# Kernel tuning notes

Measured on AMD Instinct MI355X. Metric: run time of the kernel, lower is better.

The kernel has to match this reference:

```python
import jax, jax.numpy as jnp
import numpy as np

B, S, D = 4, 2048, 1024


def setup_inputs() -> dict:
    key = jax.random.key(0)
    kq, k1, k2, k3 = jax.random.split(key, 4)
    w_scale = 1.0 / np.sqrt(D)  # ~ glorot scale for square Dense
    q = jax.random.normal(kq, (B, S, D), dtype=jnp.float32)
    Wq = jax.random.normal(k1, (D, D), dtype=jnp.float32) * w_scale
    Wk = jax.random.normal(k2, (D, D), dtype=jnp.float32) * w_scale  # unused in self-attn path (bug in original)
    Wv = jax.random.normal(k3, (D, D), dtype=jnp.float32) * w_scale
    # causal mask: 1 = masked (future), matching tf.where(mask == 1, -1e9, scores)
    mask = jnp.triu(jnp.ones((S, S), dtype=jnp.int32), k=1)
    return {"q": q, "Wq": Wq, "Wk": Wk, "Wv": Wv, "mask": mask}


def reference(q, Wq, Wk, Wv, mask):
    # Self-attention path of the original: k=None, v=None.
    WQ = jnp.einsum('bsd,de->bse', q, Wq)
    # Faithful to the original code: dense_v is applied for BOTH K and V.
    WKV = jnp.einsum('bsd,de->bse', q, Wv)
    d_k = jnp.asarray(D, dtype=q.dtype)
    scores = jnp.einsum('bqd,bkd->bqk', WQ, WKV) / jnp.sqrt(d_k)  # [B,S,S]
    scores = jnp.where(mask == 1, jnp.asarray(-1e9, scores.dtype), scores)
    attn = jax.nn.softmax(scores, axis=-1)
    return jnp.einsum('bqk,bkd->bqd', attn, WKV)
```

## Files before the change

### kernel.cpp

```cpp
#include <hip/hip_runtime.h>


typedef unsigned short u16;
typedef short short8 __attribute__((ext_vector_type(8)));
typedef float floatx4 __attribute__((ext_vector_type(4)));

#define S_LEN 2048
#define D_DIM 1024
#define BK 64

__device__ inline u16 f2b(float f) {
  unsigned u = __float_as_uint(f);
  return (u16)((u + 0x7fffu + ((u >> 16) & 1u)) >> 16);
}

__device__ __forceinline__ void gload16(const u16* g, u16* l) {
  __builtin_amdgcn_global_load_lds(
      (const __attribute__((address_space(1))) void*)g,
      (__attribute__((address_space(3))) void*)l, 16, 0, 0);
}

__global__ __launch_bounds__(256)
void cvt_f32_bf16(const float* __restrict__ src, u16* __restrict__ dst) {
  size_t idx = ((size_t)blockIdx.x * 256 + threadIdx.x) * 8;
  float4 a0 = *(const float4*)&src[idx];
  float4 a1 = *(const float4*)&src[idx + 4];
  short8 v;
  v[0] = (short)f2b(a0.x); v[1] = (short)f2b(a0.y);
  v[2] = (short)f2b(a0.z); v[3] = (short)f2b(a0.w);
  v[4] = (short)f2b(a1.x); v[5] = (short)f2b(a1.y);
  v[6] = (short)f2b(a1.z); v[7] = (short)f2b(a1.w);
  *(short8*)&dst[idx] = v;
}

__global__ __launch_bounds__(256)
void transpose_cvt2(const float* __restrict__ s0, u16* __restrict__ d0_,
                    const float* __restrict__ s1, u16* __restrict__ d1_) {
  __shared__ u16 tile[32][33];
  const float* src = blockIdx.z ? s1 : s0;
  u16* dst = blockIdx.z ? d1_ : d0_;
  int c0 = blockIdx.x * 32, r0 = blockIdx.y * 32;
  int tx = threadIdx.x, ty = threadIdx.y;
  for (int ii = 0; ii < 32; ii += 8)
    tile[ii + ty][tx] = f2b(src[(size_t)(r0 + ii + ty) * 1024 + (c0 + tx)]);
  __syncthreads();
  for (int ii = 0; ii < 32; ii += 8)
    dst[(size_t)(c0 + ii + ty) * 1024 + (r0 + tx)] = tile[tx][ii + ty];
}

__global__ __launch_bounds__(256)
void gemm_proj(const u16* __restrict__ A, const u16* __restrict__ B0,
               const u16* __restrict__ B1, u16* __restrict__ C0,
               u16* __restrict__ C1, u16* __restrict__ WKVt) {
  int id = blockIdx.x;
  int xcd = id & 7, i = id >> 3;
  int m_idx = xcd * 8 + (i & 7);
  int nz = i >> 3;
  int n0 = (nz & 7) * 128, z = nz >> 3;
  int m0 = m_idx * 128;
  const u16* Bp = z ? B1 : B0;
  u16* Cp = z ? C1 : C0;
  __shared__ __align__(16) char smem[34816];
  u16* Als = (u16*)smem;
  u16* Bls = (u16*)(smem + 16384);
  u16* Tls = (u16*)smem;
  int tid = threadIdx.x;
  int wave = tid >> 6, lane = tid & 63, quad = lane >> 4, l15 = lane & 15;
  int wm = (wave >> 1) * 64, wn = (wave & 1) * 64;
  int arow = lane >> 3;
  int acol = ((lane & 7) ^ (arow & 7)) << 3;
  floatx4 acc[4][4];
#pragma unroll
  for (int ii = 0; ii < 4; ++ii)
#pragma unroll
    for (int j = 0; j < 4; ++j) acc[ii][j] = (floatx4){0.f, 0.f, 0.f, 0.f};
  for (int kb = 0; kb < D_DIM; kb += BK) {
    __syncthreads();
#pragma unroll
    for (int p = 0; p < 4; ++p) {
      int r0 = p * 32 + wave * 8;
      gload16(&A[(size_t)(m0 + r0 + arow) * D_DIM + kb + acol], &Als[r0 * BK]);
      gload16(&Bp[(size_t)(n0 + r0 + arow) * D_DIM + kb + acol], &Bls[r0 * BK]);
    }
    __syncthreads();
#pragma unroll
    for (int kk8 = 0; kk8 < 8; kk8 += 4) {
      int cg = (((kk8 + quad) & 7) ^ (l15 & 7)) << 3;
      short8 af[4], bfr[4];
#pragma unroll
      for (int ii = 0; ii < 4; ++ii)
        af[ii] = *(const short8*)&Als[(wm + ii * 16 + l15) * BK + cg];
#pragma unroll
      for (int j = 0; j < 4; ++j)
        bfr[j] = *(const short8*)&Bls[(wn + j * 16 + l15) * BK + cg];
#pragma unroll
      for (int ii = 0; ii < 4; ++ii)
#pragma unroll
        for (int j = 0; j < 4; ++j)
          acc[ii][j] = __builtin_amdgcn_mfma_f32_16x16x32_bf16(
              af[ii], bfr[j], acc[ii][j], 0, 0, 0);
    }
  }
#pragma unroll
  for (int ii = 0; ii < 4; ++ii)
#pragma unroll
    for (int j = 0; j < 4; ++j)
#pragma unroll
      for (int r = 0; r < 4; ++r)
        Cp[(size_t)(m0 + wm + ii * 16 + quad * 4 + r) * D_DIM +
           (n0 + wn + j * 16 + l15)] = f2b(acc[ii][j][r]);
  if (z) {
    __syncthreads();
#pragma unroll
    for (int ii = 0; ii < 4; ++ii)
#pragma unroll
      for (int j = 0; j < 4; ++j)
#pragma unroll
        for (int r = 0; r < 4; ++r)
          Tls[(wn + j * 16 + l15) * 136 + (wm + ii * 16 + quad * 4 + r)] =
              f2b(acc[ii][j][r]);
    __syncthreads();
    int b = m0 >> 11, srow = m0 & 2047;
    u16* Wt = WKVt + (size_t)b * D_DIM * S_LEN;
#pragma unroll
    for (int p = 0; p < 8; ++p) {
      int e = p * 2048 + tid * 8;
      int d = e >> 7, s = e & 127;
      *(short8*)&Wt[(size_t)(n0 + d) * S_LEN + srow + s] =
          *(const short8*)&Tls[d * 136 + s];
    }
  }
}

#define GEMM64_PROLOG()                                                       \
  __shared__ u16 Als[64 * BK];                                                \
  __shared__ u16 Bls[128 * BK];                                               \
  int tid = threadIdx.x;                                                      \
  int wave = tid >> 6, lane = tid & 63, quad = lane >> 4, l15 = lane & 15;    \
  int wr = (wave >> 1) * 32, wc = (wave & 1) * 64;                            \
  int arow = lane >> 3;                                                       \
  int acol = ((lane & 7) ^ (arow & 7)) << 3;                                  \
  floatx4 acc[2][4];                                                          \
  _Pragma("unroll") for (int i = 0; i < 2; ++i)                               \
  _Pragma("unroll") for (int j = 0; j < 4; ++j)                               \
      acc[i][j] = (floatx4){0.f, 0.f, 0.f, 0.f};

#define GEMM64_KLOOP(Aptr, lda, Bptr, ldb, KEND)                              \
  for (int kb = 0; kb < (KEND); kb += BK) {                                   \
    __syncthreads();                                                          \
    _Pragma("unroll") for (int p = 0; p < 2; ++p) {                           \
      int r0 = wave * 16 + p * 8;                                             \
      gload16(&(Aptr)[(size_t)(m0 + r0 + arow) * (lda) + kb + acol],          \
              &Als[r0 * BK]);                                                 \
    }                                                                         \
    _Pragma("unroll") for (int p = 0; p < 4; ++p) {                           \
      int r0 = wave * 32 + p * 8;                                             \
      gload16(&(Bptr)[(size_t)(n0 + r0 + arow) * (ldb) + kb + acol],          \
              &Bls[r0 * BK]);                                                 \
    }                                                                         \
    __syncthreads();                                                          \
    _Pragma("unroll") for (int kk8 = 0; kk8 < 8; kk8 += 4) {                  \
      int cg = (((kk8 + quad) & 7) ^ (l15 & 7)) << 3;                         \
      short8 af[2], bfr[4];                                                   \
      _Pragma("unroll") for (int i = 0; i < 2; ++i)                           \
          af[i] = *(const short8*)&Als[(wr + i * 16 + l15) * BK + cg];        \
      _Pragma("unroll") for (int j = 0; j < 4; ++j)                           \
          bfr[j] = *(const short8*)&Bls[(wc + j * 16 + l15) * BK + cg];       \
      _Pragma("unroll") for (int i = 0; i < 2; ++i)                           \
      _Pragma("unroll") for (int j = 0; j < 4; ++j)                           \
          acc[i][j] = __builtin_amdgcn_mfma_f32_16x16x32_bf16(                \
              af[i], bfr[j], acc[i][j], 0, 0, 0);                             \
    }                                                                         \
  }

__global__ __launch_bounds__(256)
void gemm_scores(const u16* __restrict__ WQ, const u16* __restrict__ WKV,
                 u16* __restrict__ Pp, float* __restrict__ rowsum) {
  int id = blockIdx.x;
  int xcd = id & 7;
  int b = xcd & 3, h = xcd >> 2;
  int t = id >> 3;
  int m = (int)((sqrtf(8.f * (float)t + 1.f) - 1.f) * 0.5f);
  while ((m + 1) * (m + 2) / 2 <= t) ++m;
  while (m * (m + 1) / 2 > t) --m;
  int bj = t - m * (m + 1) / 2;
  int bi = 2 * m + h;
  int m0 = bi * 64, n0 = bj * 128;
  const u16* A = WQ + (size_t)b * S_LEN * D_DIM;
  const u16* Bp = WKV + (size_t)b * S_LEN * D_DIM;
  GEMM64_PROLOG();
  GEMM64_KLOOP(A, D_DIM, Bp, D_DIM, D_DIM);
  u16* Pb = Pp + (size_t)b * S_LEN * S_LEN;
  float part[2][4];
#pragma unroll
  for (int i = 0; i < 2; ++i)
#pragma unroll
    for (int r = 0; r < 4; ++r) part[i][r] = 0.f;
#pragma unroll
  for (int i = 0; i < 2; ++i)
#pragma unroll
    for (int j = 0; j < 4; ++j) {
      int col = n0 + wc + j * 16 + l15;
#pragma unroll
      for (int r = 0; r < 4; ++r) {
        int row = m0 + wr + i * 16 + quad * 4 + r;
        float p = (col > row) ? 0.f : __expf(acc[i][j][r] * 0.03125f);
        Pb[(size_t)row * S_LEN + col] = f2b(p);
        part[i][r] += p;
      }
    }
#pragma unroll
  for (int i = 0; i < 2; ++i)
#pragma unroll
    for (int r = 0; r < 4; ++r) {
      float v = part[i][r];
#pragma unroll
      for (int off = 1; off < 16; off <<= 1) v += __shfl_xor(v, off, 64);
      part[i][r] = v;
    }
  if (l15 == 0) {
#pragma unroll
    for (int i = 0; i < 2; ++i)
#pragma unroll
      for (int r = 0; r < 4; ++r)
        atomicAdd(&rowsum[b * S_LEN + m0 + wr + i * 16 + quad * 4 + r],
                  part[i][r]);
  }
}

__global__ __launch_bounds__(256)
void gemm_pv(const u16* __restrict__ Pp, const u16* __restrict__ WKVt,
             const float* __restrict__ rowsum, float* __restrict__ out) {
  int id = blockIdx.x;
  int xcd = id & 7;
  int b = xcd & 3, h = xcd >> 2;
  int r_ = id >> 3;
  int mh = 15 - (r_ >> 3);
  int bi = 2 * mh + h;
  int bj = r_ & 7;
  int m0 = bi * 64, n0 = bj * 128;
  int kend = (bi + 1) * 64;
  const u16* A = Pp + (size_t)b * S_LEN * S_LEN;
  const u16* Bp = WKVt + (size_t)b * (size_t)D_DIM * S_LEN;
  GEMM64_PROLOG();
  GEMM64_KLOOP(A, S_LEN, Bp, S_LEN, kend);
  const float* rs = rowsum + b * S_LEN;
  float* Co = out + (size_t)b * S_LEN * D_DIM;
#pragma unroll
  for (int i = 0; i < 2; ++i)
#pragma unroll
    for (int r = 0; r < 4; ++r) {
      int row = m0 + wr + i * 16 + quad * 4 + r;
      float inv = 1.0f / rs[row];
#pragma unroll
      for (int j = 0; j < 4; ++j)
        Co[(size_t)row * D_DIM + (n0 + wc + j * 16 + l15)] =
            acc[i][j][r] * inv;
    }
}

extern "C" void kernel_launch(void* const* d_in, const int* in_sizes, int n_in,
                              void* d_out, int out_size, void* d_ws, size_t ws_size,
                              hipStream_t stream) {
  const float* q = (const float*)d_in[0];
  const float* Wq = (const float*)d_in[1];
  const float* Wv = (const float*)d_in[3];
  char* ws = (char*)d_ws;
  const size_t MB = 1024 * 1024;
  u16* Wqt = (u16*)(ws);
  u16* Wvt = (u16*)(ws + 2 * MB);
  u16* qb16 = (u16*)(ws + 4 * MB);
  u16* Pp = (u16*)(ws);
  u16* WQ = (u16*)(ws + 32 * MB);
  u16* WKV = (u16*)(ws + 48 * MB);
  u16* WKVt = (u16*)(ws + 64 * MB);
  float* rowsum = (float*)(ws + 80 * MB);

  hipMemsetAsync(rowsum, 0, 4 * S_LEN * sizeof(float), stream);
  cvt_f32_bf16<<<4096, 256, 0, stream>>>(q, qb16);
  transpose_cvt2<<<dim3(32, 32, 2), dim3(32, 8), 0, stream>>>(Wq, Wqt, Wv, Wvt);
  gemm_proj<<<1024, 256, 0, stream>>>(qb16, Wqt, Wvt, WQ, WKV, WKVt);
  gemm_scores<<<1088, 256, 0, stream>>>(WQ, WKV, Pp, rowsum);
  gemm_pv<<<1024, 256, 0, stream>>>(Pp, WKVt, rowsum, (float*)d_out);
}
```

Baseline: 216.8 us.

## Rewrite projection GEMM as 256x256 8-wave tile with pipelined LDS staging

The projection GEMM moves from 128x128 tiles with 4 waves to 256x256 tiles with 8 waves (512 threads, 256 blocks). It uses a 128KB LDS buffer split into eight staged half-tiles, with loads for the next k-step issued while MFMAs on the current data run. Explicit barriers, waitcnt and setprio interleave memory and compute. The aim is more operand reuse per block and hidden global-load latency, at the cost of fewer blocks (256 across the machine, one per CU), heavy register use for the 8x4 accumulators, and a more fragile hand-written schedule.

New measurement: 232.0 us. 1.07x slower.

```diff
diff --git a/kernel.cpp b/kernel.cpp
--- a/kernel.cpp
+++ b/kernel.cpp
@@ -48,86 +48,168 @@
     dst[(size_t)(c0 + ii + ty) * 1024 + (r0 + tx)] = tile[tx][ii + ty];
 }
 
-__global__ __launch_bounds__(256)
+__global__ __launch_bounds__(512)
 void gemm_proj(const u16* __restrict__ A, const u16* __restrict__ B0,
                const u16* __restrict__ B1, u16* __restrict__ C0,
                u16* __restrict__ C1, u16* __restrict__ WKVt) {
+  __shared__ __align__(16) u16 lds[65536];
+
   int id = blockIdx.x;
-  int xcd = id & 7, i = id >> 3;
-  int m_idx = xcd * 8 + (i & 7);
-  int nz = i >> 3;
-  int n0 = (nz & 7) * 128, z = nz >> 3;
-  int m0 = m_idx * 128;
+  int xcd = id & 7, i5 = id >> 3;
+  int m_idx = xcd * 4 + (i5 & 3);
+  int n_idx = i5 >> 2;
+  int z = n_idx >> 2;
+  int n0 = (n_idx & 3) * 256;
+  int m0 = m_idx * 256;
   const u16* Bp = z ? B1 : B0;
   u16* Cp = z ? C1 : C0;
-  __shared__ __align__(16) char smem[34816];
-  u16* Als = (u16*)smem;
-  u16* Bls = (u16*)(smem + 16384);
-  u16* Tls = (u16*)smem;
+
   int tid = threadIdx.x;
-  int wave = tid >> 6, lane = tid & 63, quad = lane >> 4, l15 = lane & 15;
-  int wm = (wave >> 1) * 64, wn = (wave & 1) * 64;
-  int arow = lane >> 3;
-  int acol = ((lane & 7) ^ (arow & 7)) << 3;
-  floatx4 acc[4][4];
-#pragma unroll
-  for (int ii = 0; ii < 4; ++ii)
-#pragma unroll
-    for (int j = 0; j < 4; ++j) acc[ii][j] = (floatx4){0.f, 0.f, 0.f, 0.f};
-  for (int kb = 0; kb < D_DIM; kb += BK) {
-    __syncthreads();
-#pragma unroll
-    for (int p = 0; p < 4; ++p) {
-      int r0 = p * 32 + wave * 8;
-      gload16(&A[(size_t)(m0 + r0 + arow) * D_DIM + kb + acol], &Als[r0 * BK]);
-      gload16(&Bp[(size_t)(n0 + r0 + arow) * D_DIM + kb + acol], &Bls[r0 * BK]);
-    }
-    __syncthreads();
-#pragma unroll
-    for (int kk8 = 0; kk8 < 8; kk8 += 4) {
-      int cg = (((kk8 + quad) & 7) ^ (l15 & 7)) << 3;
-      short8 af[4], bfr[4];
-#pragma unroll
-      for (int ii = 0; ii < 4; ++ii)
-        af[ii] = *(const short8*)&Als[(wm + ii * 16 + l15) * BK + cg];
-#pragma unroll
-      for (int j = 0; j < 4; ++j)
-        bfr[j] = *(const short8*)&Bls[(wn + j * 16 + l15) * BK + cg];
-#pragma unroll
-      for (int ii = 0; ii < 4; ++ii)
-#pragma unroll
-        for (int j = 0; j < 4; ++j)
-          acc[ii][j] = __builtin_amdgcn_mfma_f32_16x16x32_bf16(
-              af[ii], bfr[j], acc[ii][j], 0, 0, 0);
-    }
-  }
-#pragma unroll
-  for (int ii = 0; ii < 4; ++ii)
-#pragma unroll
-    for (int j = 0; j < 4; ++j)
+  int wv = tid >> 6, lane = tid & 63, quad = lane >> 4, l15 = lane & 15;
+  int wm = wv >> 2, wn = wv & 3;
+
+  int off_g[2];
+#pragma unroll
+  for (int l = 0; l < 2; ++l) {
+    int chunk = (wv * 2 + l) * 64 + lane;
+    int r = chunk >> 3, cs = chunk & 7;
+    off_g[l] = r * 1024 + (cs ^ (r & 7)) * 8;
+  }
+  const u16* As0 = A + (size_t)m0 * 1024;
+  const u16* As1 = A + (size_t)(m0 + 128) * 1024;
+  const u16* Bs0 = Bp + (size_t)n0 * 1024;
+  const u16* Bs1 = Bp + (size_t)(n0 + 128) * 1024;
+
+#define PSTAGE(src, reg)                                                     \
+  {                                                                          \
+    _Pragma("unroll") for (int l = 0; l < 2; ++l)                            \
+        gload16((src) + off_g[l], &lds[(reg) * 8192 + (wv * 2 + l) * 512]);  \
+  }
+
+  int aoff[2], boff[2];
+#pragma unroll
+  for (int kk = 0; kk < 2; ++kk) {
+    int c = ((kk * 4 + quad) ^ (l15 & 7)) * 8;
+    aoff[kk] = l15 * 64 + c;
+    boff[kk] = ((wn & 1) * 64 + l15) * 64 + c;
+  }
+  const u16* A0p = &lds[(0 + wm) * 8192];
+  const u16* A1p = &lds[(4 + wm) * 8192];
+  const u16* B0p = &lds[(2 + (wn >> 1)) * 8192];
+  const u16* B1p = &lds[(6 + (wn >> 1)) * 8192];
+
+  floatx4 acc[8][4];
+#pragma unroll
+  for (int i = 0; i < 8; ++i)
+#pragma unroll
+    for (int j = 0; j < 4; ++j) acc[i][j] = (floatx4){0.f, 0.f, 0.f, 0.f};
+
+#define BARp() __builtin_amdgcn_s_barrier()
+#define WLG() asm volatile("s_waitcnt lgkmcnt(0)" ::: "memory")
+#define WVM(n) asm volatile("s_waitcnt vmcnt(" #n ")" ::: "memory")
+
+#define RDA(dst, base, fb)                                                 \
+  _Pragma("unroll") for (int f = 0; f < 4; ++f)                            \
+  _Pragma("unroll") for (int kk = 0; kk < 2; ++kk)                         \
+      dst[f][kk] = *(const short8*)&(base)[((fb) + f) * 1024 + aoff[kk]];
+#define RDB(dst, base, fb)                                                 \
+  _Pragma("unroll") for (int f = 0; f < 2; ++f)                            \
+  _Pragma("unroll") for (int kk = 0; kk < 2; ++kk)                         \
+      dst[f][kk] = *(const short8*)&(base)[((fb) + f) * 1024 + boff[kk]];
+#define MMQ(mh, nh, afq, bfq)                                              \
+  __builtin_amdgcn_s_setprio(1);                                           \
+  _Pragma("unroll") for (int f = 0; f < 4; ++f)                            \
+  _Pragma("unroll") for (int g2 = 0; g2 < 2; ++g2)                         \
+  _Pragma("unroll") for (int kk = 0; kk < 2; ++kk)                         \
+      acc[(mh) * 4 + f][(nh) * 2 + g2] =                                   \
+          __builtin_amdgcn_mfma_f32_16x16x32_bf16(                         \
+              afq[f][kk], bfq[g2][kk], acc[(mh) * 4 + f][(nh) * 2 + g2],   \
+              0, 0, 0);                                                    \
+  __builtin_amdgcn_s_setprio(0);
+
+  PSTAGE(As0, 0); PSTAGE(As1, 1); PSTAGE(Bs0, 2); PSTAGE(Bs1, 3);
+  PSTAGE(As0 + 64, 4); PSTAGE(As1 + 64, 5);
+  WVM(4);
+  BARp();
+
+#pragma unroll 1
+  for (int it = 0; it < 8; ++it) {
+    int kb = it * 128;
+    short8 af0[4][2], af1[4][2], bf0[2][2], bf1[2][2];
+    RDA(af0, A0p, 0); RDB(bf0, B0p, 0);
+    PSTAGE(Bs0 + kb + 64, 6);
+    BARp(); WLG();
+    MMQ(0, 0, af0, bf0);
+    BARp();
+    RDA(af1, A0p, 4); RDB(bf1, B0p, 2);
+    PSTAGE(Bs1 + kb + 64, 7);
+    BARp(); WLG();
+    MMQ(1, 1, af1, bf1);
+    BARp();
+    if (it < 7) PSTAGE(As0 + kb + 128, 0);
+    BARp();
+    MMQ(0, 1, af0, bf1);
+    BARp();
+    if (it < 7) PSTAGE(As1 + kb + 128, 1);
+    BARp();
+    MMQ(1, 0, af1, bf0);
+    if (it < 7) { WVM(4); } else { WVM(0); }
+    BARp();
+    RDA(af0, A1p, 0); RDB(bf0, B1p, 0);
+    if (it < 7) PSTAGE(Bs0 + kb + 128, 2);
+    BARp(); WLG();
+    MMQ(0, 0, af0, bf0);
+    BARp();
+    RDA(af1, A1p, 4); RDB(bf1, B1p, 2);
+    if (it < 7) PSTAGE(Bs1 + kb + 128, 3);
+    BARp(); WLG();
+    MMQ(1, 1, af1, bf1);
+    BARp();
+    if (it < 7) PSTAGE(As0 + kb + 192, 4);
+    BARp();
+    MMQ(0, 1, af0, bf1);
+    BARp();
+    if (it < 7) PSTAGE(As1 + kb + 192, 5);
+    BARp();
+    MMQ(1, 0, af1, bf0);
+    if (it < 7) WVM(4);
+    BARp();
+  }
+
+  asm volatile("s_waitcnt vmcnt(0) lgkmcnt(0)" ::: "memory");
+#pragma unroll
+  for (int mf = 0; mf < 8; ++mf)
+#pragma unroll
+    for (int nf = 0; nf < 4; ++nf)
 #pragma unroll
       for (int r = 0; r < 4; ++r)
-        Cp[(size_t)(m0 + wm + ii * 16 + quad * 4 + r) * D_DIM +
-           (n0 + wn + j * 16 + l15)] = f2b(acc[ii][j][r]);
+        Cp[(size_t)(m0 + wm * 128 + mf * 16 + quad * 4 + r) * D_DIM +
+           (n0 + wn * 64 + nf * 16 + l15)] = f2b(acc[mf][nf][r]);
+
   if (z) {
-    __syncthreads();
-#pragma unroll
-    for (int ii = 0; ii < 4; ++ii)
-#pragma unroll
-      for (int j = 0; j < 4; ++j)
-#pragma unroll
-        for (int r = 0; r < 4; ++r)
-          Tls[(wn + j * 16 + l15) * 136 + (wm + ii * 16 + quad * 4 + r)] =
-              f2b(acc[ii][j][r]);
-    __syncthreads();
     int b = m0 >> 11, srow = m0 & 2047;
     u16* Wt = WKVt + (size_t)b * D_DIM * S_LEN;
 #pragma unroll
-    for (int p = 0; p < 8; ++p) {
-      int e = p * 2048 + tid * 8;
-      int d = e >> 7, s = e & 127;
-      *(short8*)&Wt[(size_t)(n0 + d) * S_LEN + srow + s] =
-          *(const short8*)&Tls[d * 136 + s];
+    for (int ph = 0; ph < 2; ++ph) {
+      BARp();
+      if ((wn >> 1) == ph) {
+#pragma unroll
+        for (int mf = 0; mf < 8; ++mf)
+#pragma unroll
+          for (int nf = 0; nf < 4; ++nf)
+#pragma unroll
+            for (int r = 0; r < 4; ++r)
+              lds[((wn & 1) * 64 + nf * 16 + l15) * 272 +
+                  (wm * 128 + mf * 16 + quad * 4 + r)] = f2b(acc[mf][nf][r]);
+      }
+      BARp();
+#pragma unroll
+      for (int rr = 0; rr < 8; ++rr) {
+        int idx = rr * 512 + tid;
+        int dl = idx >> 5, sc = idx & 31;
+        *(short8*)&Wt[(size_t)(n0 + ph * 128 + dl) * S_LEN + srow + sc * 8] =
+            *(const short8*)&lds[dl * 272 + sc * 8];
+      }
     }
   }
 }
@@ -279,7 +361,7 @@
   hipMemsetAsync(rowsum, 0, 4 * S_LEN * sizeof(float), stream);
   cvt_f32_bf16<<<4096, 256, 0, stream>>>(q, qb16);
   transpose_cvt2<<<dim3(32, 32, 2), dim3(32, 8), 0, stream>>>(Wq, Wqt, Wv, Wvt);
-  gemm_proj<<<1024, 256, 0, stream>>>(qb16, Wqt, Wvt, WQ, WKV, WKVt);
+  gemm_proj<<<256, 512, 0, stream>>>(qb16, Wqt, Wvt, WQ, WKV, WKVt);
   gemm_scores<<<1088, 256, 0, stream>>>(WQ, WKV, Pp, rowsum);
   gemm_pv<<<1024, 256, 0, stream>>>(Pp, WKVt, rowsum, (float*)d_out);
 }
```
